# Optimization experiments

Measured on AMD Instinct MI355X. Metric: run time of the kernel, lower is better.

Reference implementation:

```python
import jax, jax.numpy as jnp
import numpy as np

EPS = 1e-12
SIMILARITY = 'dot'  # non-tensor forward arg, closed over


def setup_inputs() -> dict:
    key = jax.random.key(0)
    k1, k2, k3, k4 = jax.random.split(key, 4)
    N, M, D = 4096, 8192, 512
    x = jax.random.normal(k1, (N, D), dtype=jnp.float32)
    x_n = jax.random.normal(k2, (M, D), dtype=jnp.float32)
    # Linear(D, 3) params
    W = jax.random.normal(k3, (3, D), dtype=jnp.float32) * (1.0 / np.sqrt(D))
    bias = jax.random.normal(k4, (3,), dtype=jnp.float32) * 0.01
    return {"x": x, "x_n": x_n, "W": W, "bias": bias}


def _sim_matrix(x, x_n, similarity):
    if similarity == 'l2':
        d2 = (jnp.sum(x * x, 1)[:, None] - 2.0 * (x @ x_n.T)
              + jnp.sum(x_n * x_n, 1)[None, :])
        return -jnp.sqrt(jnp.maximum(d2, 0.0))
    elif similarity == 'l1':
        return -jnp.sum(jnp.abs(x[:, None, :] - x_n[None, :, :]), axis=-1)
    elif similarity == 'dot':
        return (x @ x_n.T) / x.shape[1]
    elif similarity == 'cos':
        xn = x / jnp.linalg.norm(x, axis=1, keepdims=True)
        yn = x_n / jnp.linalg.norm(x_n, axis=1, keepdims=True)
        return xn @ yn.T


def reference(x, x_n, W, bias):
    # pointwise params from a Linear(D,3)+Sigmoid head, clamped to (eps, 1-eps)
    p = jnp.clip(jax.nn.sigmoid(x @ W.T + bias), EPS, 1.0 - EPS)  # [N,3]
    a = p[:, 0:1]
    b = p[:, 1:2]
    s = p[:, 2:3]
    b = a + b * (1.0 - a)

    sim = _sim_matrix(x, x_n, SIMILARITY)                # [N,M]
    smin = jnp.min(sim, axis=1, keepdims=True)
    smax = jnp.max(sim, axis=1, keepdims=True)
    sim_norm = (sim - smin) / (smax - smin)

    # x != x_n -> plain row max (torch.equal branch is False)
    top_sims = jnp.max(sim_norm, axis=1, keepdims=True)  # [N,1]
    a = jnp.minimum(a, top_sims) - EPS

    num = jnp.maximum(jnp.abs(sim_norm - a) ** (1.0 / s), EPS)
    denom = num + jnp.maximum(jnp.abs(b - sim_norm) ** (1.0 / s), EPS)
    soft_mask = num / denom

    lo = sim_norm < a
    hi = sim_norm > b
    soft_mask = jnp.where(lo, 0.0, jnp.where(hi, 1.0, soft_mask))
    # safe log: masked-to-0 entries give -inf forward, zero grad (matches torch)
    safe = jnp.where(lo, 1.0, soft_mask)
    log_mask = jnp.where(lo, -jnp.inf, jnp.log(safe))
    return sim + log_mask
```

## Files before the change

kernel.cpp:

```cpp
#include <hip/hip_runtime.h>
#include <hip/hip_fp16.h>
#include <math.h>

#define EPSF 1e-12f
#define NEG_HUGE (-1e30f)

typedef _Float16 half8_t __attribute__((ext_vector_type(8)));
typedef _Float16 half4_t __attribute__((ext_vector_type(4)));
typedef float floatx4 __attribute__((ext_vector_type(4)));

__device__ __forceinline__ float sigmoid_stable(float v) {
    if (v >= 0.0f) {
        return 1.0f / (1.0f + expf(-v));
    } else {
        float e = expf(v);
        return e / (1.0f + e);
    }
}

__global__ __launch_bounds__(64) void row_params_kernel(
    const float* __restrict__ x, const float* __restrict__ W,
    const float* __restrict__ bias,
    float* __restrict__ aeff, float* __restrict__ bnew, float* __restrict__ tinv)
{
    const int r = blockIdx.x;
    const int l = threadIdx.x;
    const float* xr = x + (size_t)r * 512;
    float s0 = 0.0f, s1 = 0.0f, s2 = 0.0f;
#pragma unroll
    for (int i = 0; i < 8; ++i) {
        int e = l * 8 + i;
        float xv = xr[e];
        s0 = fmaf(xv, W[e], s0);
        s1 = fmaf(xv, W[512 + e], s1);
        s2 = fmaf(xv, W[1024 + e], s2);
    }
#pragma unroll
    for (int off = 32; off > 0; off >>= 1) {
        s0 += __shfl_xor(s0, off);
        s1 += __shfl_xor(s1, off);
        s2 += __shfl_xor(s2, off);
    }
    if (l == 0) {
        float p0 = fminf(fmaxf(sigmoid_stable(s0 + bias[0]), EPSF), 1.0f);
        float p1 = fminf(fmaxf(sigmoid_stable(s1 + bias[1]), EPSF), 1.0f);
        float p2 = fminf(fmaxf(sigmoid_stable(s2 + bias[2]), EPSF), 1.0f);
        float b = p0 + p1 * (1.0f - p0);
        float ae = fminf(p0, 1.0f) - EPSF;
        aeff[r] = ae;
        bnew[r] = b;
        tinv[r] = 1.0f / p2;
    }
}

__global__ __launch_bounds__(256) void split_both_kernel(
    const float* __restrict__ x, const float* __restrict__ xn,
    _Float16* __restrict__ A2, _Float16* __restrict__ B2)
{
    int idx = blockIdx.x * 256 + threadIdx.x;
    int row = idx >> 7;
    int c = (idx & 127) << 2;
    const float* src;
    _Float16* dst;
    bool isB;
    if (row < 4096) {
        src = x + (size_t)row * 512 + c;
        dst = A2 + (size_t)row * 1536 + c;
        isB = false;
    } else {
        int r = row - 4096;
        src = xn + (size_t)r * 512 + c;
        dst = B2 + (size_t)r * 1536 + c;
        isB = true;
    }
    float4 v = *(const float4*)src;
    _Float16 h0 = (_Float16)v.x, h1 = (_Float16)v.y,
             h2 = (_Float16)v.z, h3 = (_Float16)v.w;
    half4_t hv = {h0, h1, h2, h3};
    half4_t lv = {(_Float16)(v.x - (float)h0), (_Float16)(v.y - (float)h1),
                  (_Float16)(v.z - (float)h2), (_Float16)(v.w - (float)h3)};
    *(half4_t*)(dst) = hv;
    *(half4_t*)(dst + 512)  = isB ? lv : hv;
    *(half4_t*)(dst + 1024) = isB ? hv : lv;
}

#define VMW_(N) asm volatile("s_waitcnt vmcnt(" #N ")" ::: "memory")
#define VMW(N) VMW_(N)
#define BARR() asm volatile("s_barrier" ::: "memory")
#define LGKM0() asm volatile("s_waitcnt lgkmcnt(0)" ::: "memory")

__device__ __forceinline__ void gload16(const _Float16* g, _Float16* l) {
    __builtin_amdgcn_global_load_lds(
        (const __attribute__((address_space(1))) unsigned int*)g,
        (__attribute__((address_space(3))) unsigned int*)l, 16, 0, 0);
}

#define PHASE(FMB, STAGES, VMN, DOREADB, Q)                                    \
    {                                                                          \
        if (DOREADB) {                                                         \
            const _Float16* bb = lds + (Q) * 16384 + BrdW;                     \
            _Pragma("unroll")                                                  \
            for (int fn = 0; fn < 4; ++fn) {                                   \
                bfr[fn][0] = *(const half8_t*)(bb + fn * 1024 + g0);           \
                bfr[fn][1] = *(const half8_t*)(bb + fn * 1024 + g1);           \
            }                                                                  \
        }                                                                      \
        const _Float16* ab = lds + (Q) * 16384 + ArdW;                         \
        half8_t af0k0 = *(const half8_t*)(ab + (FMB) * 1024 + g0);             \
        half8_t af0k1 = *(const half8_t*)(ab + (FMB) * 1024 + g1);             \
        half8_t af1k0 = *(const half8_t*)(ab + ((FMB) + 1) * 1024 + g0);       \
        half8_t af1k1 = *(const half8_t*)(ab + ((FMB) + 1) * 1024 + g1);       \
        STAGES;                                                                \
        BARR();                                                                \
        LGKM0();                                                               \
        __builtin_amdgcn_s_setprio(1);                                         \
        _Pragma("unroll")                                                      \
        for (int fn = 0; fn < 4; ++fn) {                                       \
            acc[FMB][fn] = __builtin_amdgcn_mfma_f32_16x16x32_f16(             \
                af0k0, bfr[fn][0], acc[FMB][fn], 0, 0, 0);                     \
            acc[FMB][fn] = __builtin_amdgcn_mfma_f32_16x16x32_f16(             \
                af0k1, bfr[fn][1], acc[FMB][fn], 0, 0, 0);                     \
            acc[(FMB) + 1][fn] = __builtin_amdgcn_mfma_f32_16x16x32_f16(       \
                af1k0, bfr[fn][0], acc[(FMB) + 1][fn], 0, 0, 0);               \
            acc[(FMB) + 1][fn] = __builtin_amdgcn_mfma_f32_16x16x32_f16(       \
                af1k1, bfr[fn][1], acc[(FMB) + 1][fn], 0, 0, 0);               \
        }                                                                      \
        __builtin_amdgcn_s_setprio(0);                                         \
        VMW(VMN);                                                              \
        BARR();                                                                \
    }

__global__ __launch_bounds__(512) void mfma_gemm256_kernel(
    const _Float16* __restrict__ A, const _Float16* __restrict__ B,
    float* __restrict__ C,
    float* __restrict__ pmin, float* __restrict__ pmax)
{
    constexpr int KP = 1536;
    constexpr int NN = 8192;
    constexpr int NT = KP / 64;
    __shared__ __align__(16) _Float16 lds[65536];

    const int tid = threadIdx.x;
    const int wave = tid >> 6, lane = tid & 63;
    const int bx = blockIdx.x;
    const int by = blockIdx.y;
    const int wm = (wave >> 2) * 128;
    const int wn = (wave & 3) * 64;

    const int rl = lane & 15, lq = lane >> 4;
    const int rx7 = lane & 7;
    const int lrow = lane >> 3, gph = lane & 7;
    const int glog = gph ^ lrow;

    const _Float16* Bg = B + (size_t)(bx * 256 + wave * 8 + lrow) * KP + glog * 8;
    const _Float16* Ag = A + (size_t)(by * 256 + ((wave & 4) ? 128 : 0)
                                      + (wave & 3) * 8 + lrow) * KP + glog * 8;
    const int BdstW = 32768 + (wave * 8) * 64;
    const int AdstW = (((wave & 4) ? 128 : 0) + (wave & 3) * 8) * 64;
    const int ArdW = (wm + rl) * 64;
    const int BrdW = 32768 + (wn + rl) * 64;
    const int g0 = (lq ^ rx7) * 8;
    const int g1 = ((4 + lq) ^ rx7) * 8;

    floatx4 acc[8][4] = {};
    half8_t bfr[4][2];

    auto stageB = [&](int u, int qn, int kn) {
        gload16(Bg + (size_t)u * (64 * KP) + kn * 64,
                lds + qn * 16384 + BdstW + u * 4096);
    };
    auto stageA = [&](int s, int qn, int kn) {
        gload16(Ag + (size_t)s * (32 * KP) + kn * 64,
                lds + qn * 16384 + AdstW + s * 2048);
    };

#pragma unroll
    for (int u = 0; u < 4; ++u) stageB(u, 0, 0);
#pragma unroll
    for (int s = 0; s < 4; ++s) stageA(s, 0, 0);
    VMW(3);
    BARR();

    for (int kt = 0; kt < NT - 1; ++kt) {
        const int q = kt & 1, qn = q ^ 1, kn = kt + 1;
        PHASE(0, (stageB(0, qn, kn), stageB(1, qn, kn)), 4, true, q);
        PHASE(2, (stageB(2, qn, kn), stageB(3, qn, kn)), 5, false, q);
        PHASE(4, (stageA(0, qn, kn), stageA(1, qn, kn)), 6, false, q);
        PHASE(6, (stageA(2, qn, kn), stageA(3, qn, kn)), 3, false, q);
    }
    PHASE(0, (void)0, 2, true, 1);
    PHASE(2, (void)0, 1, false, 1);
    PHASE(4, (void)0, 0, false, 1);
    PHASE(6, (void)0, 63, false, 1);

    const float sc = 1.0f / 512.0f;
    const int row0 = by * 256 + wm + lq * 4;
    const int col0 = bx * 256 + wn + rl;
    const int pslot = bx * 4 + (wave & 3);
#pragma unroll
    for (int fm = 0; fm < 8; ++fm) {
        float mn[4], mx[4];
#pragma unroll
        for (int r = 0; r < 4; ++r) {
            float* cp = C + (size_t)(row0 + fm * 16 + r) * NN + col0;
            float v0 = acc[fm][0][r] * sc, v1 = acc[fm][1][r] * sc;
            float v2 = acc[fm][2][r] * sc, v3 = acc[fm][3][r] * sc;
            cp[0] = v0; cp[16] = v1; cp[32] = v2; cp[48] = v3;
            mn[r] = fminf(fminf(v0, v1), fminf(v2, v3));
            mx[r] = fmaxf(fmaxf(v0, v1), fmaxf(v2, v3));
        }
#pragma unroll
        for (int off = 1; off < 16; off <<= 1)
#pragma unroll
            for (int r = 0; r < 4; ++r) {
                mn[r] = fminf(mn[r], __shfl_xor(mn[r], off));
                mx[r] = fmaxf(mx[r], __shfl_xor(mx[r], off));
            }
        if (rl == 0) {
#pragma unroll
            for (int r = 0; r < 4; ++r) {
                size_t row = (size_t)(row0 + fm * 16 + r);
                pmin[(row << 7) + pslot] = mn[r];
                pmax[(row << 7) + pslot] = mx[r];
            }
        }
    }
}

__global__ __launch_bounds__(64) void minmax_reduce_kernel(
    const float* __restrict__ pmin, const float* __restrict__ pmax,
    float* __restrict__ smin, float* __restrict__ smax)
{
    const int r = blockIdx.x;
    const int l = threadIdx.x;
    const float* bmin = pmin + ((size_t)r << 7);
    const float* bmax = pmax + ((size_t)r << 7);
    float mn = fminf(bmin[l], bmin[l + 64]);
    float mx = fmaxf(bmax[l], bmax[l + 64]);
#pragma unroll
    for (int off = 32; off > 0; off >>= 1) {
        mn = fminf(mn, __shfl_xor(mn, off));
        mx = fmaxf(mx, __shfl_xor(mx, off));
    }
    if (l == 0) {
        smin[r] = mn;
        smax[r] = mx;
    }
}

#define BM 128
#define BN 128
#define BK 16
__global__ __launch_bounds__(256) void sgemm_nt_kernel(
    const float* __restrict__ A, const float* __restrict__ B,
    float* __restrict__ C)
{
    const int K = 512;
    const int N = 8192;
    __shared__ float As[BK][BM];
    __shared__ float Bs[BK][BN];
    const int t = threadIdx.x;
    const int bx = blockIdx.x, by = blockIdx.y;
    const int m0 = t >> 2;
    const int kq = (t & 3) << 2;
    const float* Ap = A + ((size_t)(by * BM + m0) * K + kq);
    const float* Bp = B + ((size_t)(bx * BN + m0) * K + kq);
    const int tx = t & 15, ty = t >> 4;
    float acc[8][8] = {};
    float4 a0 = *(const float4*)(Ap), a1 = *(const float4*)(Ap + (size_t)64 * K);
    float4 b0 = *(const float4*)(Bp), b1 = *(const float4*)(Bp + (size_t)64 * K);
    for (int kt = 0; kt < K / BK; ++kt) {
        As[kq + 0][m0] = a0.x; As[kq + 1][m0] = a0.y; As[kq + 2][m0] = a0.z; As[kq + 3][m0] = a0.w;
        As[kq + 0][m0 + 64] = a1.x; As[kq + 1][m0 + 64] = a1.y; As[kq + 2][m0 + 64] = a1.z; As[kq + 3][m0 + 64] = a1.w;
        Bs[kq + 0][m0] = b0.x; Bs[kq + 1][m0] = b0.y; Bs[kq + 2][m0] = b0.z; Bs[kq + 3][m0] = b0.w;
        Bs[kq + 0][m0 + 64] = b1.x; Bs[kq + 1][m0 + 64] = b1.y; Bs[kq + 2][m0 + 64] = b1.z; Bs[kq + 3][m0 + 64] = b1.w;
        __syncthreads();
        if (kt + 1 < K / BK) {
            const float* Ap2 = Ap + (size_t)(kt + 1) * BK;
            const float* Bp2 = Bp + (size_t)(kt + 1) * BK;
            a0 = *(const float4*)(Ap2); a1 = *(const float4*)(Ap2 + (size_t)64 * K);
            b0 = *(const float4*)(Bp2); b1 = *(const float4*)(Bp2 + (size_t)64 * K);
        }
#pragma unroll
        for (int k = 0; k < BK; ++k) {
            float4 xa0 = *(const float4*)(&As[k][ty * 8]);
            float4 xa1 = *(const float4*)(&As[k][ty * 8 + 4]);
            float4 yb0 = *(const float4*)(&Bs[k][tx * 8]);
            float4 yb1 = *(const float4*)(&Bs[k][tx * 8 + 4]);
            float av[8] = {xa0.x, xa0.y, xa0.z, xa0.w, xa1.x, xa1.y, xa1.z, xa1.w};
            float bv[8] = {yb0.x, yb0.y, yb0.z, yb0.w, yb1.x, yb1.y, yb1.z, yb1.w};
#pragma unroll
            for (int i = 0; i < 8; ++i)
#pragma unroll
                for (int j = 0; j < 8; ++j)
                    acc[i][j] = fmaf(av[i], bv[j], acc[i][j]);
        }
        __syncthreads();
    }
    const float sc = 1.0f / 512.0f;
    const int gm = by * BM + ty * 8, gn = bx * BN + tx * 8;
#pragma unroll
    for (int i = 0; i < 8; ++i) {
        float4 o0 = make_float4(acc[i][0] * sc, acc[i][1] * sc, acc[i][2] * sc, acc[i][3] * sc);
        float4 o1 = make_float4(acc[i][4] * sc, acc[i][5] * sc, acc[i][6] * sc, acc[i][7] * sc);
        float* cp = C + (size_t)(gm + i) * N + gn;
        *(float4*)(cp) = o0;
        *(float4*)(cp + 4) = o1;
    }
}

__global__ __launch_bounds__(256) void row_minmax_kernel(
    const float* __restrict__ C, float* __restrict__ smin, float* __restrict__ smax)
{
    const int r = blockIdx.x;
    const float4* row = (const float4*)(C + (size_t)r * 8192);
    float mn = INFINITY, mx = -INFINITY;
#pragma unroll
    for (int i = 0; i < 8; ++i) {
        float4 v = row[threadIdx.x + i * 256];
        mn = fminf(mn, fminf(fminf(v.x, v.y), fminf(v.z, v.w)));
        mx = fmaxf(mx, fmaxf(fmaxf(v.x, v.y), fmaxf(v.z, v.w)));
    }
#pragma unroll
    for (int off = 32; off > 0; off >>= 1) {
        mn = fminf(mn, __shfl_xor(mn, off));
        mx = fmaxf(mx, __shfl_xor(mx, off));
    }
    __shared__ float smn[4], smx[4];
    if ((threadIdx.x & 63) == 0) {
        smn[threadIdx.x >> 6] = mn;
        smx[threadIdx.x >> 6] = mx;
    }
    __syncthreads();
    if (threadIdx.x == 0) {
        mn = fminf(fminf(smn[0], smn[1]), fminf(smn[2], smn[3]));
        mx = fmaxf(fmaxf(smx[0], smx[1]), fmaxf(smx[2], smx[3]));
        smin[r] = mn;
        smax[r] = mx;
    }
}

__device__ __forceinline__ float fast_pow(float x, float t) {
    return __expf(t * __logf(x));
}

__global__ __launch_bounds__(256) void epilogue_kernel(
    float* __restrict__ C,
    const float* __restrict__ aeff, const float* __restrict__ bnew,
    const float* __restrict__ tinv,
    const float* __restrict__ smin, const float* __restrict__ smax)
{
    const int r = blockIdx.y;
    const int c4 = blockIdx.x * 256 + threadIdx.x;
    const float a = aeff[r];
    const float b = bnew[r];
    const float t = tinv[r];
    const float mn = smin[r];
    const float range = smax[r] - mn;
    const float inv_range = (range > 0.0f) ? (1.0f / range) : 0.0f;

    floatx4* p = (floatx4*)(C + (size_t)r * 8192) + c4;
    floatx4 v = __builtin_nontemporal_load(p);
    floatx4 out;
#pragma unroll
    for (int i = 0; i < 4; ++i) {
        float sim = v[i];
        float sn = (sim - mn) * inv_range;
        float lm;
        if (sn < a) {
            lm = NEG_HUGE;
        } else if (sn > b) {
            lm = 0.0f;
        } else {
            float num = fmaxf(fast_pow(fabsf(sn - a), t), EPSF);
            float den = num + fmaxf(fast_pow(fabsf(b - sn), t), EPSF);
            lm = __logf(num / den);
        }
        out[i] = sim + lm;
    }
    __builtin_nontemporal_store(out, p);
}

extern "C" void kernel_launch(void* const* d_in, const int* in_sizes, int n_in,
                              void* d_out, int out_size, void* d_ws, size_t ws_size,
                              hipStream_t stream)
{
    const float* x    = (const float*)d_in[0];
    const float* x_n  = (const float*)d_in[1];
    const float* W    = (const float*)d_in[2];
    const float* bias = (const float*)d_in[3];
    float* C = (float*)d_out;
    float* ws = (float*)d_ws;

    float* aeff = ws;
    float* bnew = ws + 4096;
    float* tinv = ws + 8192;
    float* smin = ws + 12288;
    float* smax = ws + 16384;

    const size_t pmin_off = 128 * 1024;
    const size_t pbytes = (size_t)4096 * 128 * 4;
    const size_t a2_off = pmin_off + 2 * pbytes;
    const size_t a2_bytes = (size_t)4096 * 1536 * 2;
    const size_t b2_off = a2_off + a2_bytes;
    const size_t need = b2_off + (size_t)8192 * 1536 * 2;

    row_params_kernel<<<4096, 64, 0, stream>>>(x, W, bias, aeff, bnew, tinv);

    if (ws_size >= need) {
        float* pmin = (float*)((char*)d_ws + pmin_off);
        float* pmax = (float*)((char*)d_ws + pmin_off + pbytes);
        _Float16* A2 = (_Float16*)((char*)d_ws + a2_off);
        _Float16* B2 = (_Float16*)((char*)d_ws + b2_off);
        split_both_kernel<<<6144, 256, 0, stream>>>(x, x_n, A2, B2);
        mfma_gemm256_kernel<<<dim3(32, 16), 512, 0, stream>>>(A2, B2, C, pmin, pmax);
        minmax_reduce_kernel<<<4096, 64, 0, stream>>>(pmin, pmax, smin, smax);
    } else {
        sgemm_nt_kernel<<<dim3(8192 / BN, 4096 / BM), 256, 0, stream>>>(x, x_n, C);
        row_minmax_kernel<<<4096, 256, 0, stream>>>(C, smin, smax);
    }

    epilogue_kernel<<<dim3(8, 4096), 256, 0, stream>>>(C, aeff, bnew, tinv,
                                                       smin, smax);
}
```

Baseline: 297.1 us.

## Software-pipeline LDS fragment reads one phase ahead of MFMAs in GEMM loop

Restructures the GEMM main loop so the A and B fragments for the next phase are read from LDS into alternate register sets while the current phase's MFMAs execute. This removes the explicit lgkmcnt(0) wait before each MFMA group. The loop is unrolled by two k-tiles with ping-pong B buffers, and a launch-bounds occupancy hint of 2 is added. The extra fragment registers raise VGPR pressure and could cause spills under the tighter occupancy bound.

```diff
diff --git a/kernel.cpp b/kernel.cpp
--- a/kernel.cpp
+++ b/kernel.cpp
@@ -86,8 +86,7 @@
 
 #define VMW_(N) asm volatile("s_waitcnt vmcnt(" #N ")" ::: "memory")
 #define VMW(N) VMW_(N)
-#define BARR() asm volatile("s_barrier" ::: "memory")
-#define LGKM0() asm volatile("s_waitcnt lgkmcnt(0)" ::: "memory")
+#define BARR() __builtin_amdgcn_s_barrier()
 
 __device__ __forceinline__ void gload16(const _Float16* g, _Float16* l) {
     __builtin_amdgcn_global_load_lds(
@@ -95,49 +94,41 @@
         (__attribute__((address_space(3))) unsigned int*)l, 16, 0, 0);
 }
 
-#define PHASE(FMB, STAGES, VMN, DOREADB, Q)                                    \
-    {                                                                          \
-        if (DOREADB) {                                                         \
-            const _Float16* bb = lds + (Q) * 16384 + BrdW;                     \
-            _Pragma("unroll")                                                  \
-            for (int fn = 0; fn < 4; ++fn) {                                   \
-                bfr[fn][0] = *(const half8_t*)(bb + fn * 1024 + g0);           \
-                bfr[fn][1] = *(const half8_t*)(bb + fn * 1024 + g1);           \
-            }                                                                  \
-        }                                                                      \
-        const _Float16* ab = lds + (Q) * 16384 + ArdW;                         \
-        half8_t af0k0 = *(const half8_t*)(ab + (FMB) * 1024 + g0);             \
-        half8_t af0k1 = *(const half8_t*)(ab + (FMB) * 1024 + g1);             \
-        half8_t af1k0 = *(const half8_t*)(ab + ((FMB) + 1) * 1024 + g0);       \
-        half8_t af1k1 = *(const half8_t*)(ab + ((FMB) + 1) * 1024 + g1);       \
-        STAGES;                                                                \
-        BARR();                                                                \
-        LGKM0();                                                               \
-        __builtin_amdgcn_s_setprio(1);                                         \
-        _Pragma("unroll")                                                      \
-        for (int fn = 0; fn < 4; ++fn) {                                       \
-            acc[FMB][fn] = __builtin_amdgcn_mfma_f32_16x16x32_f16(             \
-                af0k0, bfr[fn][0], acc[FMB][fn], 0, 0, 0);                     \
-            acc[FMB][fn] = __builtin_amdgcn_mfma_f32_16x16x32_f16(             \
-                af0k1, bfr[fn][1], acc[FMB][fn], 0, 0, 0);                     \
-            acc[(FMB) + 1][fn] = __builtin_amdgcn_mfma_f32_16x16x32_f16(       \
-                af1k0, bfr[fn][0], acc[(FMB) + 1][fn], 0, 0, 0);               \
-            acc[(FMB) + 1][fn] = __builtin_amdgcn_mfma_f32_16x16x32_f16(       \
-                af1k1, bfr[fn][1], acc[(FMB) + 1][fn], 0, 0, 0);               \
-        }                                                                      \
-        __builtin_amdgcn_s_setprio(0);                                         \
-        VMW(VMN);                                                              \
-        BARR();                                                                \
-    }
-
-__global__ __launch_bounds__(512) void mfma_gemm256_kernel(
+#define RD_A4(dst, QQ, qd)                                                      \
+    dst[0] = *(const half8_t*)(lds + (QQ)*16384 + ArdW + (2*(qd))*1024 + g0);   \
+    dst[1] = *(const half8_t*)(lds + (QQ)*16384 + ArdW + (2*(qd))*1024 + g1);   \
+    dst[2] = *(const half8_t*)(lds + (QQ)*16384 + ArdW + (2*(qd)+1)*1024 + g0); \
+    dst[3] = *(const half8_t*)(lds + (QQ)*16384 + ArdW + (2*(qd)+1)*1024 + g1);
+
+#define RD_B8(dst, QQ)                                                          \
+    _Pragma("unroll")                                                           \
+    for (int fn = 0; fn < 4; ++fn) {                                            \
+        dst[2*fn]   = *(const half8_t*)(lds + (QQ)*16384 + BrdW + fn*1024 + g0);\
+        dst[2*fn+1] = *(const half8_t*)(lds + (QQ)*16384 + BrdW + fn*1024 + g1);\
+    }
+
+#define MFMA_Q(qd, af, bf)                                                      \
+    __builtin_amdgcn_s_setprio(1);                                              \
+    _Pragma("unroll")                                                           \
+    for (int fn = 0; fn < 4; ++fn) {                                            \
+        acc[2*(qd)][fn] = __builtin_amdgcn_mfma_f32_16x16x32_f16(               \
+            af[0], bf[2*fn], acc[2*(qd)][fn], 0, 0, 0);                         \
+        acc[2*(qd)][fn] = __builtin_amdgcn_mfma_f32_16x16x32_f16(               \
+            af[1], bf[2*fn+1], acc[2*(qd)][fn], 0, 0, 0);                       \
+        acc[2*(qd)+1][fn] = __builtin_amdgcn_mfma_f32_16x16x32_f16(             \
+            af[2], bf[2*fn], acc[2*(qd)+1][fn], 0, 0, 0);                       \
+        acc[2*(qd)+1][fn] = __builtin_amdgcn_mfma_f32_16x16x32_f16(             \
+            af[3], bf[2*fn+1], acc[2*(qd)+1][fn], 0, 0, 0);                     \
+    }                                                                           \
+    __builtin_amdgcn_s_setprio(0);
+
+__global__ __launch_bounds__(512, 2) void mfma_gemm256_kernel(
     const _Float16* __restrict__ A, const _Float16* __restrict__ B,
     float* __restrict__ C,
     float* __restrict__ pmin, float* __restrict__ pmax)
 {
     constexpr int KP = 1536;
     constexpr int NN = 8192;
-    constexpr int NT = KP / 64;
     __shared__ __align__(16) _Float16 lds[65536];
 
     const int tid = threadIdx.x;
@@ -163,7 +154,7 @@
     const int g1 = ((4 + lq) ^ rx7) * 8;
 
     floatx4 acc[8][4] = {};
-    half8_t bfr[4][2];
+    half8_t a0[4], a1[4], bA[8], bB[8];
 
     auto stageB = [&](int u, int qn, int kn) {
         gload16(Bg + (size_t)u * (64 * KP) + kn * 64,
@@ -180,18 +171,43 @@
     for (int s = 0; s < 4; ++s) stageA(s, 0, 0);
     VMW(3);
     BARR();
-
-    for (int kt = 0; kt < NT - 1; ++kt) {
-        const int q = kt & 1, qn = q ^ 1, kn = kt + 1;
-        PHASE(0, (stageB(0, qn, kn), stageB(1, qn, kn)), 4, true, q);
-        PHASE(2, (stageB(2, qn, kn), stageB(3, qn, kn)), 5, false, q);
-        PHASE(4, (stageA(0, qn, kn), stageA(1, qn, kn)), 6, false, q);
-        PHASE(6, (stageA(2, qn, kn), stageA(3, qn, kn)), 3, false, q);
-    }
-    PHASE(0, (void)0, 2, true, 1);
-    PHASE(2, (void)0, 1, false, 1);
-    PHASE(4, (void)0, 0, false, 1);
-    PHASE(6, (void)0, 63, false, 1);
+    RD_B8(bA, 0); RD_A4(a0, 0, 0);
+    stageB(0, 1, 1); stageB(1, 1, 1);
+    VMW(4);
+    BARR();
+
+    for (int kt = 0; kt < 22; kt += 2) {
+        const int k1 = kt + 1, k2 = kt + 2, k3 = kt + 3;
+        RD_A4(a1, 0, 1); stageB(2, 1, k1); stageB(3, 1, k1);
+        MFMA_Q(0, a0, bA); VMW(5); BARR();
+        RD_A4(a0, 0, 2); stageA(0, 1, k1); stageA(1, 1, k1);
+        MFMA_Q(1, a1, bA); VMW(6); BARR();
+        RD_A4(a1, 0, 3); stageA(2, 1, k1); stageA(3, 1, k1);
+        MFMA_Q(2, a0, bA); VMW(3); BARR();
+        RD_B8(bB, 1); RD_A4(a0, 1, 0); stageB(0, 0, k2); stageB(1, 0, k2);
+        MFMA_Q(3, a1, bA); VMW(4); BARR();
+        RD_A4(a1, 1, 1); stageB(2, 0, k2); stageB(3, 0, k2);
+        MFMA_Q(0, a0, bB); VMW(5); BARR();
+        RD_A4(a0, 1, 2); stageA(0, 0, k2); stageA(1, 0, k2);
+        MFMA_Q(1, a1, bB); VMW(6); BARR();
+        RD_A4(a1, 1, 3); stageA(2, 0, k2); stageA(3, 0, k2);
+        MFMA_Q(2, a0, bB); VMW(3); BARR();
+        RD_B8(bA, 0); RD_A4(a0, 0, 0); stageB(0, 1, k3); stageB(1, 1, k3);
+        MFMA_Q(3, a1, bB); VMW(4); BARR();
+    }
+
+    RD_A4(a1, 0, 1); stageB(2, 1, 23); stageB(3, 1, 23);
+    MFMA_Q(0, a0, bA); VMW(5); BARR();
+    RD_A4(a0, 0, 2); stageA(0, 1, 23); stageA(1, 1, 23);
+    MFMA_Q(1, a1, bA); VMW(6); BARR();
+    RD_A4(a1, 0, 3); stageA(2, 1, 23); stageA(3, 1, 23);
+    MFMA_Q(2, a0, bA); VMW(3); BARR();
+    RD_B8(bB, 1); RD_A4(a0, 1, 0);
+    MFMA_Q(3, a1, bA); VMW(2); BARR();
+    RD_A4(a1, 1, 1); MFMA_Q(0, a0, bB); VMW(1); BARR();
+    RD_A4(a0, 1, 2); MFMA_Q(1, a1, bB); VMW(0); BARR();
+    RD_A4(a1, 1, 3); MFMA_Q(2, a0, bB);
+    MFMA_Q(3, a1, bB);
 
     const float sc = 1.0f / 512.0f;
     const int row0 = by * 256 + wm + lq * 4;
```

Result: no change. 295.6 us (-0.5%).
